# Performance work log

Measured on AMD Instinct MI355X. Metric: run time of the kernel, lower is better.

The kernel has to match this reference:

```python
import jax, jax.numpy as jnp
import numpy as np
from jax import lax

FREQ, TIME = 8, 8
TSLOTS, NUM_AP = 8, 4
N_DEV = 8192
E_DD, E_DA, E_AD = 262144, 32768, 32768
HID = 64


def _w(key, shape):
    fan_in = shape[0] if len(shape) == 2 else int(np.prod(shape[1:]))
    return jax.random.normal(key, shape, jnp.float32) / np.sqrt(fan_in)


def setup_inputs() -> dict:
    key = jax.random.key(0)
    ks = iter(jax.random.split(key, 64))
    inp = {}
    inp['device_pos'] = jax.random.normal(next(ks), (N_DEV, 2), jnp.float32)
    inp['ap_pos'] = jax.random.normal(next(ks), (NUM_AP, 2), jnp.float32)
    inp['csi'] = jax.random.normal(next(ks), (N_DEV, NUM_AP, FREQ, TIME, 2), jnp.float32)
    inp['node_packets'] = jax.random.randint(next(ks), (N_DEV,), 0, 100, jnp.int32)
    inp['dd_src'] = jax.random.randint(next(ks), (E_DD,), 0, N_DEV, jnp.int32)
    inp['dd_dst'] = jax.random.randint(next(ks), (E_DD,), 0, N_DEV, jnp.int32)
    inp['da_src'] = jax.random.randint(next(ks), (E_DA,), 0, N_DEV, jnp.int32)
    inp['da_dst'] = jax.random.randint(next(ks), (E_DA,), 0, NUM_AP, jnp.int32)
    inp['ad_src'] = jax.random.randint(next(ks), (E_AD,), 0, NUM_AP, jnp.int32)
    inp['ad_dst'] = jax.random.randint(next(ks), (E_AD,), 0, N_DEV, jnp.int32)
    # CSIEncoder params
    inp['cnn1_W'] = _w(next(ks), (16, 2, 3, 3)); inp['cnn1_b'] = jnp.zeros((16,), jnp.float32)
    inp['cnn2_W'] = _w(next(ks), (32, 16, 3, 3)); inp['cnn2_b'] = jnp.zeros((32,), jnp.float32)
    inp['csi_fc_W'] = _w(next(ks), (32 * FREQ * TIME, HID)); inp['csi_fc_b'] = jnp.zeros((HID,), jnp.float32)
    # DeviceEncoder params
    inp['dev_pos_W'] = _w(next(ks), (3, 16)); inp['dev_pos_b'] = jnp.zeros((16,), jnp.float32)
    inp['dev_csi_W'] = _w(next(ks), (NUM_AP * HID, 64)); inp['dev_csi_b'] = jnp.zeros((64,), jnp.float32)
    inp['dev_merge_W'] = _w(next(ks), (80, 64)); inp['dev_merge_b'] = jnp.zeros((64,), jnp.float32)
    # APEncoder params
    inp['ap_enc_W'] = _w(next(ks), (2, 64)); inp['ap_enc_b'] = jnp.zeros((64,), jnp.float32)
    # 2 hetero layers x 3 relations GraphConv(64,64)
    for name in ['g1_dd', 'g1_da', 'g1_ad', 'g2_dd', 'g2_da', 'g2_ad']:
        inp[name + '_W'] = _w(next(ks), (64, 64))
        inp[name + '_b'] = jnp.zeros((64,), jnp.float32)
    # ap_head (sched_head is defined but unused in the original forward)
    inp['aph1_W'] = _w(next(ks), (64, 64)); inp['aph1_b'] = jnp.zeros((64,), jnp.float32)
    inp['aph2_W'] = _w(next(ks), (64, TSLOTS * NUM_AP)); inp['aph2_b'] = jnp.zeros((TSLOTS * NUM_AP,), jnp.float32)
    return inp


def _conv2d(x, W, b):
    y = lax.conv_general_dilated(x, W, (1, 1), 'SAME', dimension_numbers=('NCHW', 'OIHW', 'NCHW'))
    return y + b[None, :, None, None]


def _graph_conv(x_src, src, dst, n_src, n_dst, W, b):
    # DGL GraphConv, norm='both': x/sqrt(out_deg) -> scatter-sum -> /sqrt(in_deg) -> linear
    ones = jnp.ones(src.shape[0], x_src.dtype)
    deg_out = jnp.maximum(jax.ops.segment_sum(ones, src, num_segments=n_src), 1.0)
    deg_in = jnp.maximum(jax.ops.segment_sum(ones, dst, num_segments=n_dst), 1.0)
    m = (x_src * lax.rsqrt(deg_out)[:, None])[src]            # gather per edge
    agg = jax.ops.segment_sum(m, dst, num_segments=n_dst)      # scatter-sum to dst
    agg = agg * lax.rsqrt(deg_in)[:, None]
    return agg @ W + b


def reference(device_pos, ap_pos, csi, node_packets, dd_src, dd_dst, da_src, da_dst, ad_src, ad_dst,
              cnn1_W, cnn1_b, cnn2_W, cnn2_b, csi_fc_W, csi_fc_b,
              dev_pos_W, dev_pos_b, dev_csi_W, dev_csi_b, dev_merge_W, dev_merge_b,
              ap_enc_W, ap_enc_b,
              g1_dd_W, g1_dd_b, g1_da_W, g1_da_b, g1_ad_W, g1_ad_b,
              g2_dd_W, g2_dd_b, g2_da_W, g2_da_b, g2_ad_W, g2_ad_b,
              aph1_W, aph1_b, aph2_W, aph2_b):
    N, AP = csi.shape[0], csi.shape[1]
    # CSIEncoder (per-AP loop vectorized as a single batched conv over N*AP)
    x = csi.reshape(N * AP, FREQ, TIME, 2).transpose(0, 3, 1, 2)   # [N*AP,2,F,T]
    x = jax.nn.relu(_conv2d(x, cnn1_W, cnn1_b))
    x = jax.nn.relu(_conv2d(x, cnn2_W, cnn2_b))
    x = x.reshape(N * AP, -1)                                      # [N*AP, 32*F*T]
    csi_embed = jax.nn.relu(x @ csi_fc_W + csi_fc_b).reshape(N, AP * HID)
    # DeviceEncoder
    pin = jnp.concatenate([device_pos, node_packets.astype(jnp.float32)[:, None]], axis=1)
    pos_f = jax.nn.relu(pin @ dev_pos_W + dev_pos_b)
    csi_f = jax.nn.relu(csi_embed @ dev_csi_W + dev_csi_b)
    h_dev = jax.nn.relu(jnp.concatenate([pos_f, csi_f], axis=1) @ dev_merge_W + dev_merge_b)
    # APEncoder
    h_ap = jax.nn.relu(ap_pos @ ap_enc_W + ap_enc_b)
    # HeteroGraphConv layer 1 (aggregate='sum' across relations sharing dst type)
    hd1 = (_graph_conv(h_dev, dd_src, dd_dst, N, N, g1_dd_W, g1_dd_b)
           + _graph_conv(h_ap, ad_src, ad_dst, NUM_AP, N, g1_ad_W, g1_ad_b))
    ha1 = _graph_conv(h_dev, da_src, da_dst, N, NUM_AP, g1_da_W, g1_da_b)
    hd1, ha1 = jax.nn.relu(hd1), jax.nn.relu(ha1)
    # HeteroGraphConv layer 2
    hd2 = (_graph_conv(hd1, dd_src, dd_dst, N, N, g2_dd_W, g2_dd_b)
           + _graph_conv(ha1, ad_src, ad_dst, NUM_AP, N, g2_ad_W, g2_ad_b))
    hd2 = jax.nn.relu(hd2)
    # ap_head -> [N, T, A]
    ap_logits = (jax.nn.relu(hd2 @ aph1_W + aph1_b) @ aph2_W + aph2_b).reshape(N, TSLOTS, NUM_AP)
    logits_AP = ap_logits.transpose(2, 1, 0)                       # [A,T,N]
    # eval branch: deterministic softmax + argmax one-hot over devices
    ap_soft_AP = jax.nn.softmax(logits_AP, axis=-1)
    idx = jnp.argmax(logits_AP, axis=-1)                           # [A,T]
    ap_onehot_AP = jax.nn.one_hot(idx, N, dtype=logits_AP.dtype)   # [A,T,N]
    ap_onehot_final = ap_onehot_AP.transpose(2, 1, 0)              # [N,T,A]
    sched_soft = ap_soft_AP.sum(axis=0).T                          # [N,T]
    sched_hard = (ap_onehot_final.sum(axis=-1) > 0).astype(jnp.float32)
    return (sched_hard, ap_logits, sched_soft)
```

## Files before the change

kernel.cpp:

```cpp
#include <hip/hip_runtime.h>

#define NDEV 8192
#define NAP  4
#define NSAMP 32768
#define EDD 262144
#define EDA 32768
#define EAD 32768
#define KC 128
#define ASTR2 132

typedef float vf2 __attribute__((ext_vector_type(2)));
static __device__ __forceinline__ vf2 pk_fma(vf2 a, vf2 b, vf2 c) {
    return __builtin_elementwise_fma(a, b, c);
}

using sh8 = __attribute__((ext_vector_type(8))) short;
using f32x4 = __attribute__((ext_vector_type(4))) float;
using f32x16 = __attribute__((ext_vector_type(16))) float;

static __device__ __forceinline__ unsigned short bf16_rtne(float f) {
    unsigned u = __float_as_uint(f);
    u += 0x7fffu + ((u >> 16) & 1u);
    return (unsigned short)(u >> 16);
}
static __device__ __forceinline__ float bf16f(unsigned short h) {
    return __uint_as_float(((unsigned)h) << 16);
}

__global__ void repack_kernel(const float* __restrict__ w2, float* __restrict__ wpk,
                              const float* __restrict__ w1, float* __restrict__ w1p,
                              const float* __restrict__ fcW, uint4* __restrict__ wfc,
                              const float* __restrict__ Wc, uint4* __restrict__ wcc)
{
    int i = blockIdx.x * 256 + threadIdx.x;
    if (i < 1152) {
        int lane = i & 63, s = (i >> 6) & 1, tap = i >> 7;
        int oc = lane & 31, g = lane >> 5;
        unsigned int d[4];
        #pragma unroll
        for (int d4 = 0; d4 < 4; ++d4) {
            unsigned short u01[2];
            #pragma unroll
            for (int h = 0; h < 2; ++h) {
                int e = 2 * d4 + h;
                int ic = g * 8 + e;
                float v = w2[oc * 144 + ic * 9 + tap];
                unsigned short hi = bf16_rtne(v);
                u01[h] = (s == 0) ? hi : bf16_rtne(v - bf16f(hi));
            }
            d[d4] = (unsigned)u01[0] | ((unsigned)u01[1] << 16);
        }
        ((uint4*)wpk)[i] = make_uint4(d[0], d[1], d[2], d[3]);
    }
    int j = i - 4608;
    if (j >= 0 && j < 288) {
        int h = j & 1, v = j >> 1;
        int o2 = v & 7, r = v >> 3;
        w1p[j] = w1[(2 * o2 + h) * 18 + r];
    }
    int h1 = i - 5120;
    if (h1 >= 0 && h1 < 32768) {
        int s = h1 & 1, l = (h1 >> 1) & 63, nt = (h1 >> 7) & 3, kstep = h1 >> 9;
        unsigned int d[4];
        #pragma unroll
        for (int d4 = 0; d4 < 4; ++d4) {
            unsigned short u01[2];
            #pragma unroll
            for (int hh = 0; hh < 2; ++hh) {
                int e = 2 * d4 + hh;
                int kp = kstep * 32 + (l >> 4) * 8 + e;
                int korig = (kp & 31) * 64 + (kp >> 5);
                int n = nt * 16 + (l & 15);
                float v = fcW[(long)korig * 64 + n];
                unsigned short hi = bf16_rtne(v);
                u01[hh] = (s == 0) ? hi : bf16_rtne(v - bf16f(hi));
            }
            d[d4] = (unsigned)u01[0] | ((unsigned)u01[1] << 16);
        }
        wfc[h1] = make_uint4(d[0], d[1], d[2], d[3]);
    }
    int h2 = i - 37888;
    if (h2 >= 0 && h2 < 4096) {
        int s = h2 & 1, l = (h2 >> 1) & 63, nt = (h2 >> 7) & 3, kstep = h2 >> 9;
        unsigned int d[4];
        #pragma unroll
        for (int d4 = 0; d4 < 4; ++d4) {
            unsigned short u01[2];
            #pragma unroll
            for (int hh = 0; hh < 2; ++hh) {
                int e = 2 * d4 + hh;
                int k = kstep * 32 + (l >> 4) * 8 + e;
                int n = nt * 16 + (l & 15);
                float v = Wc[(long)k * 64 + n];
                unsigned short hi = bf16_rtne(v);
                u01[hh] = (s == 0) ? hi : bf16_rtne(v - bf16f(hi));
            }
            d[d4] = (unsigned)u01[0] | ((unsigned)u01[1] << 16);
        }
        wcc[h2] = make_uint4(d[0], d[1], d[2], d[3]);
    }
}

#define C2STR 2052
__global__ __launch_bounds__(512) void convfc_kernel(
    const float* __restrict__ csi,
    const float* __restrict__ w1p, const float* __restrict__ b1,
    const float* __restrict__ wpk, const float* __restrict__ b2,
    const uint4* __restrict__ wfc, const float* __restrict__ fcb,
    float* __restrict__ emb)
{
    __shared__ __align__(16) char smem[135680];
    __shared__ float sw1p[288];
    __shared__ float sb1[16];
    __shared__ float sb2[32];
    __shared__ float sbF[64];
    float* inpad = (float*)smem;
    unsigned short* c1h = (unsigned short*)(smem + 12800);
    float* c2h = (float*)smem;
    float* red = (float*)smem;
    const int tid = threadIdx.x;
    const int lane = tid & 63;
    const int w = __builtin_amdgcn_readfirstlane(tid >> 6);

    for (int i = tid; i < 288; i += 512) sw1p[i] = w1p[i];
    if (tid < 16) sb1[tid] = b1[tid];
    if (tid < 32) sb2[tid] = b2[tid];
    if (tid < 64) sbF[tid] = fcb[tid];
    {
        const uint4 z4 = make_uint4(0u, 0u, 0u, 0u);
        uint4* ip4 = (uint4*)inpad;
        for (int i = tid; i < 800; i += 512) ip4[i] = z4;
        uint4* c14 = (uint4*)c1h;
        for (int i = tid; i < 15360; i += 512) c14[i] = z4;
    }
    __syncthreads();

    const long s0 = (long)blockIdx.x * 16;
    for (int i = tid; i < 2048; i += 512) {
        int si = i >> 7, r = i & 127;
        int f = r >> 4, t = (r >> 1) & 7, c = r & 1;
        inpad[si * 200 + c * 100 + (f + 1) * 10 + (t + 1)] = csi[s0 * 128 + i];
    }
    __syncthreads();

    #pragma unroll
    for (int it = 0; it < 2; ++it) {
        const int si1 = it * 8 + w;
        const int p1 = lane;
        const int f1 = p1 >> 3, t1 = p1 & 7;
        float inv[18];
        #pragma unroll
        for (int ic = 0; ic < 2; ++ic)
            #pragma unroll
            for (int df = 0; df < 3; ++df)
                #pragma unroll
                for (int dt = 0; dt < 3; ++dt)
                    inv[ic * 9 + df * 3 + dt] =
                        inpad[si1 * 200 + ic * 100 + (f1 + df) * 10 + (t1 + dt)];
        vf2 a1[8];
        #pragma unroll
        for (int o2 = 0; o2 < 8; ++o2) a1[o2] = (vf2){sb1[2 * o2], sb1[2 * o2 + 1]};
        const vf2* sw1v = (const vf2*)sw1p;
        #pragma unroll
        for (int r = 0; r < 18; ++r) {
            vf2 xv = {inv[r], inv[r]};
            #pragma unroll
            for (int o2 = 0; o2 < 8; ++o2)
                a1[o2] = pk_fma(xv, sw1v[r * 8 + o2], a1[o2]);
        }
        float v[16];
        #pragma unroll
        for (int o2 = 0; o2 < 8; ++o2) {
            v[2 * o2]     = fmaxf(a1[o2].x, 0.f);
            v[2 * o2 + 1] = fmaxf(a1[o2].y, 0.f);
        }
        const int cell = ((f1 + 1) * 12 + (t1 + 1)) * 8;
        #pragma unroll
        for (int g = 0; g < 2; ++g) {
            unsigned int hd[4], ld[4];
            #pragma unroll
            for (int d = 0; d < 4; ++d) {
                float x0 = v[g * 8 + 2 * d], x1 = v[g * 8 + 2 * d + 1];
                unsigned short h0 = bf16_rtne(x0), h1 = bf16_rtne(x1);
                unsigned short l0 = bf16_rtne(x0 - bf16f(h0));
                unsigned short l1 = bf16_rtne(x1 - bf16f(h1));
                hd[d] = (unsigned)h0 | ((unsigned)h1 << 16);
                ld[d] = (unsigned)l0 | ((unsigned)l1 << 16);
            }
            *(uint4*)&c1h[(si1 * 4 + g) * 960 + cell]     = make_uint4(hd[0], hd[1], hd[2], hd[3]);
            *(uint4*)&c1h[(si1 * 4 + 2 + g) * 960 + cell] = make_uint4(ld[0], ld[1], ld[2], ld[3]);
        }
    }

    sh8 Bh[9], Bl[9];
    {
        const sh8* bfp = (const sh8*)wpk;
        #pragma unroll
        for (int tap = 0; tap < 9; ++tap) {
            Bh[tap] = bfp[(tap * 2 + 0) * 64 + lane];
            Bl[tap] = bfp[(tap * 2 + 1) * 64 + lane];
        }
    }
    __syncthreads();

    const int rr = lane & 31, g = lane >> 5;
    const float bias2 = sb2[rr];
    const int p0f = rr >> 3, pt = rr & 7;
    const int p1f = 4 + p0f;
    #pragma unroll
    for (int q = 0; q < 2; ++q) {
        const int s = q * 8 + w;
        f32x16 acc0, acc1;
        #pragma unroll
        for (int u = 0; u < 16; ++u) { acc0[u] = bias2; acc1[u] = bias2; }
        const int hb = (s * 4 + g) * 960;
        const int lb = (s * 4 + 2 + g) * 960;
        #pragma unroll
        for (int df = 0; df < 3; ++df) {
            #pragma unroll
            for (int dt = 0; dt < 3; ++dt) {
                const int tap = df * 3 + dt;
                const int c0 = ((p0f + df) * 12 + (pt + dt)) * 8;
                const int c1i = ((p1f + df) * 12 + (pt + dt)) * 8;
                sh8 Ah0 = *(const sh8*)&c1h[hb + c0];
                sh8 Al0 = *(const sh8*)&c1h[lb + c0];
                sh8 Ah1 = *(const sh8*)&c1h[hb + c1i];
                sh8 Al1 = *(const sh8*)&c1h[lb + c1i];
                acc0 = __builtin_amdgcn_mfma_f32_32x32x16_bf16(Ah0, Bh[tap], acc0, 0, 0, 0);
                acc1 = __builtin_amdgcn_mfma_f32_32x32x16_bf16(Ah1, Bh[tap], acc1, 0, 0, 0);
                acc0 = __builtin_amdgcn_mfma_f32_32x32x16_bf16(Ah0, Bl[tap], acc0, 0, 0, 0);
                acc1 = __builtin_amdgcn_mfma_f32_32x32x16_bf16(Ah1, Bl[tap], acc1, 0, 0, 0);
                acc0 = __builtin_amdgcn_mfma_f32_32x32x16_bf16(Al0, Bh[tap], acc0, 0, 0, 0);
                acc1 = __builtin_amdgcn_mfma_f32_32x32x16_bf16(Al1, Bh[tap], acc1, 0, 0, 0);
            }
        }
        __syncthreads();
        float* crow = c2h + (size_t)s * C2STR;
        #pragma unroll
        for (int i = 0; i < 16; ++i) {
            const int pos = (i & 3) + 8 * (i >> 2) + 4 * g;
            crow[pos * 32 + rr]        = fmaxf(acc0[i], 0.f);
            crow[(pos + 32) * 32 + rr] = fmaxf(acc1[i], 0.f);
        }
    }
    __syncthreads();

    const int ks = w;
    const int mrow = lane & 15;
    const int g2 = lane >> 4;
    f32x4 acc[4];
    #pragma unroll
    for (int nt = 0; nt < 4; ++nt) acc[nt] = (f32x4){0.f, 0.f, 0.f, 0.f};
    #pragma unroll 2
    for (int t = 0; t < 8; ++t) {
        const int kstep = ks * 8 + t;
        const uint4* bp = wfc + (size_t)kstep * 512 + lane * 2;
        uint4 bh0 = bp[0],   bl0 = bp[1];
        uint4 bh1 = bp[128], bl1 = bp[129];
        uint4 bh2 = bp[256], bl2 = bp[257];
        uint4 bh3 = bp[384], bl3 = bp[385];
        const float4 a0 = *(const float4*)&c2h[mrow * C2STR + kstep * 32 + g2 * 8];
        const float4 a1 = *(const float4*)&c2h[mrow * C2STR + kstep * 32 + g2 * 8 + 4];
        float av[8] = {a0.x, a0.y, a0.z, a0.w, a1.x, a1.y, a1.z, a1.w};
        unsigned short hs[8], lss[8];
        #pragma unroll
        for (int e = 0; e < 8; ++e) {
            hs[e] = bf16_rtne(av[e]);
            lss[e] = bf16_rtne(av[e] - bf16f(hs[e]));
        }
        sh8 Ah = {(short)hs[0], (short)hs[1], (short)hs[2], (short)hs[3],
                  (short)hs[4], (short)hs[5], (short)hs[6], (short)hs[7]};
        sh8 Al = {(short)lss[0], (short)lss[1], (short)lss[2], (short)lss[3],
                  (short)lss[4], (short)lss[5], (short)lss[6], (short)lss[7]};
        #define FCMM(ntv, bhv, blv) \
            acc[ntv] = __builtin_amdgcn_mfma_f32_16x16x32_bf16(Ah, *(const sh8*)&(bhv), acc[ntv], 0, 0, 0); \
            acc[ntv] = __builtin_amdgcn_mfma_f32_16x16x32_bf16(Ah, *(const sh8*)&(blv), acc[ntv], 0, 0, 0); \
            acc[ntv] = __builtin_amdgcn_mfma_f32_16x16x32_bf16(Al, *(const sh8*)&(bhv), acc[ntv], 0, 0, 0);
        FCMM(0, bh0, bl0)
        FCMM(1, bh1, bl1)
        FCMM(2, bh2, bl2)
        FCMM(3, bh3, bl3)
        #undef FCMM
    }
    __syncthreads();
    #pragma unroll
    for (int nt = 0; nt < 4; ++nt)
        #pragma unroll
        for (int r = 0; r < 4; ++r)
            red[(ks * 16 + g2 * 4 + r) * 64 + nt * 16 + mrow] = acc[nt][r];
    __syncthreads();
    if (tid < 256) {
        const int m = tid >> 4, oq = tid & 15;
        float4 sum;
        sum.x = sbF[oq * 4 + 0]; sum.y = sbF[oq * 4 + 1];
        sum.z = sbF[oq * 4 + 2]; sum.w = sbF[oq * 4 + 3];
        #pragma unroll
        for (int jq = 0; jq < 8; ++jq) {
            float4 rv = *(float4*)&red[(jq * 16 + m) * 64 + oq * 4];
            sum.x += rv.x; sum.y += rv.y; sum.z += rv.z; sum.w += rv.w;
        }
        float4 o4;
        o4.x = fmaxf(sum.x, 0.f); o4.y = fmaxf(sum.y, 0.f);
        o4.z = fmaxf(sum.z, 0.f); o4.w = fmaxf(sum.w, 0.f);
        *(float4*)&emb[(s0 + m) * 64 + oq * 4] = o4;
    }
}

__global__ __launch_bounds__(256) void fc16_kernel(
    const float* __restrict__ A, const uint4* __restrict__ Wfrag,
    const float* __restrict__ bias, float* __restrict__ out, int K)
{
    __shared__ __align__(16) float smem[4224];
    float* As = smem;
    const int tid = threadIdx.x;
    const long m0g = (long)blockIdx.x * 16;
    const int ks = tid >> 6;
    const int lane = tid & 63;
    const int mrow = lane & 15;
    const int g = lane >> 4;

    f32x4 acc[4];
    #pragma unroll
    for (int nt = 0; nt < 4; ++nt) acc[nt] = (f32x4){0.f, 0.f, 0.f, 0.f};

    for (int kc = 0; kc < K; kc += KC) {
        __syncthreads();
        #pragma unroll
        for (int i = 0; i < 2; ++i) {
            int idx = tid + i * 256;
            int m = idx >> 5, kq = idx & 31;
            float4 v = *(const float4*)&A[(m0g + m) * K + kc + kq * 4];
            *(float4*)&As[m * ASTR2 + kq * 4] = v;
        }
        __syncthreads();
        const int kstep = (kc >> 5) + ks;
        const uint4* bp = Wfrag + (size_t)kstep * 512 + lane * 2;
        uint4 bh0 = bp[0],   bl0 = bp[1];
        uint4 bh1 = bp[128], bl1 = bp[129];
        uint4 bh2 = bp[256], bl2 = bp[257];
        uint4 bh3 = bp[384], bl3 = bp[385];
        const float4 a0 = *(const float4*)&As[mrow * ASTR2 + ks * 32 + g * 8];
        const float4 a1 = *(const float4*)&As[mrow * ASTR2 + ks * 32 + g * 8 + 4];
        float av[8] = {a0.x, a0.y, a0.z, a0.w, a1.x, a1.y, a1.z, a1.w};
        unsigned short hs[8], lss[8];
        #pragma unroll
        for (int e = 0; e < 8; ++e) {
            hs[e] = bf16_rtne(av[e]);
            lss[e] = bf16_rtne(av[e] - bf16f(hs[e]));
        }
        sh8 Ah = {(short)hs[0], (short)hs[1], (short)hs[2], (short)hs[3],
                  (short)hs[4], (short)hs[5], (short)hs[6], (short)hs[7]};
        sh8 Al = {(short)lss[0], (short)lss[1], (short)lss[2], (short)lss[3],
                  (short)lss[4], (short)lss[5], (short)lss[6], (short)lss[7]};
        #define FCMM(ntv, bhv, blv) \
            acc[ntv] = __builtin_amdgcn_mfma_f32_16x16x32_bf16(Ah, *(const sh8*)&(bhv), acc[ntv], 0, 0, 0); \
            acc[ntv] = __builtin_amdgcn_mfma_f32_16x16x32_bf16(Ah, *(const sh8*)&(blv), acc[ntv], 0, 0, 0); \
            acc[ntv] = __builtin_amdgcn_mfma_f32_16x16x32_bf16(Al, *(const sh8*)&(bhv), acc[ntv], 0, 0, 0);
        FCMM(0, bh0, bl0)
        FCMM(1, bh1, bl1)
        FCMM(2, bh2, bl2)
        FCMM(3, bh3, bl3)
        #undef FCMM
    }
    __syncthreads();
    float* red = smem;
    #pragma unroll
    for (int nt = 0; nt < 4; ++nt)
        #pragma unroll
        for (int r = 0; r < 4; ++r)
            red[(ks * 16 + g * 4 + r) * 64 + nt * 16 + mrow] = acc[nt][r];
    __syncthreads();
    {
        int m = tid >> 4, oq = tid & 15;
        float4 r0 = *(float4*)&red[(0 * 16 + m) * 64 + oq * 4];
        float4 r1 = *(float4*)&red[(1 * 16 + m) * 64 + oq * 4];
        float4 r2 = *(float4*)&red[(2 * 16 + m) * 64 + oq * 4];
        float4 r3 = *(float4*)&red[(3 * 16 + m) * 64 + oq * 4];
        const float4 b4 = *(const float4*)&bias[oq * 4];
        float4 o4;
        o4.x = fmaxf(r0.x + r1.x + r2.x + r3.x + b4.x, 0.f);
        o4.y = fmaxf(r0.y + r1.y + r2.y + r3.y + b4.y, 0.f);
        o4.z = fmaxf(r0.z + r1.z + r2.z + r3.z + b4.z, 0.f);
        o4.w = fmaxf(r0.w + r1.w + r2.w + r3.w + b4.w, 0.f);
        *(float4*)&out[(m0g + m) * 64 + oq * 4] = o4;
    }
}

__global__ __launch_bounds__(256) void merge_kernel(
    const float* __restrict__ dpos, const int* __restrict__ pkts,
    const float* __restrict__ csif,
    const float* __restrict__ Wp, const float* __restrict__ bp,
    const float* __restrict__ Wm, const float* __restrict__ bm,
    const int* __restrict__ degout,
    float* __restrict__ hdev, float* __restrict__ xn,
    const float* __restrict__ appos, const float* __restrict__ Wap,
    const float* __restrict__ bap, const int* __restrict__ degapo,
    float* __restrict__ hap, float* __restrict__ xnap)
{
    __shared__ float sWm[80][64];
    __shared__ float spos[4][16];
    __shared__ float scf[4][64];
    const int tid = threadIdx.x;
    for (int i = tid; i < 5120; i += 256) sWm[i >> 6][i & 63] = Wm[i];
    const int n0 = blockIdx.x * 4;
    (&scf[0][0])[tid] = csif[(long)n0 * 64 + tid];
    if (tid < 64) {
        int dl = tid >> 4, o = tid & 15;
        int d = n0 + dl;
        float px = dpos[d * 2], py = dpos[d * 2 + 1], pk = (float)pkts[d];
        float v = bp[o] + px * Wp[o] + py * Wp[16 + o] + pk * Wp[32 + o];
        spos[dl][o] = fmaxf(v, 0.f);
    }
    __syncthreads();
    const int o = tid & 63, dl = tid >> 6;
    float h = bm[o];
    #pragma unroll
    for (int j = 0; j < 16; ++j) h += spos[dl][j] * sWm[j][o];
    #pragma unroll 8
    for (int j = 0; j < 64; ++j) h += scf[dl][j] * sWm[16 + j][o];
    h = fmaxf(h, 0.f);
    const long idx = (long)(n0 + dl) * 64 + o;
    hdev[idx] = h;
    xn[idx] = h * rsqrtf(fmaxf((float)degout[n0 + dl], 1.f));
    if (blockIdx.x == 0) {
        int a = tid >> 6, oo = tid & 63;
        float v = fmaxf(bap[oo] + appos[a * 2] * Wap[oo] + appos[a * 2 + 1] * Wap[64 + oo], 0.f);
        hap[tid] = v;
        xnap[tid] = v * rsqrtf(fmaxf((float)degapo[a], 1.f));
    }
}

__global__ __launch_bounds__(256) void degrees_kernel(
    const int* __restrict__ dd_src, const int* __restrict__ dd_dst,
    const int* __restrict__ da_src, const int* __restrict__ da_dst,
    const int* __restrict__ ad_src, const int* __restrict__ ad_dst,
    int* deg_dd_out, int* deg_dd_in, int* deg_da_out, int* deg_ad_in, int* deg_small)
{
    __shared__ int s4[16];
    const int tid = threadIdx.x;
    if (tid < 16) s4[tid] = 0;
    __syncthreads();
    const int gid = blockIdx.x * 256 + tid;
    atomicAdd(&deg_dd_out[dd_src[gid]], 1);
    atomicAdd(&deg_dd_in[dd_dst[gid]], 1);
    if (gid < EDA) {
        atomicAdd(&deg_da_out[da_src[gid]], 1);
        atomicAdd(&s4[da_dst[gid]], 1);
        atomicAdd(&s4[8 + ad_src[gid]], 1);
        atomicAdd(&deg_ad_in[ad_dst[gid]], 1);
    }
    __syncthreads();
    if (tid < 16 && s4[tid] != 0) atomicAdd(&deg_small[tid], s4[tid]);
}

__global__ __launch_bounds__(1024) void scan_kernel(
    const int* __restrict__ degA, int* rsA, int* curA,
    const int* __restrict__ degB, int* rsB, int* curB)
{
    const int* deg = blockIdx.x ? degB : degA;
    int* rs = blockIdx.x ? rsB : rsA;
    int* cur = blockIdx.x ? curB : curA;
    __shared__ int sd[1024];
    const int tid = threadIdx.x;
    const int base = tid * 8;
    int v[8]; int s = 0;
    #pragma unroll
    for (int j = 0; j < 8; ++j) { v[j] = deg[base + j]; s += v[j]; }
    sd[tid] = s;
    __syncthreads();
    for (int off = 1; off < 1024; off <<= 1) {
        int t = (tid >= off) ? sd[tid - off] : 0;
        __syncthreads();
        sd[tid] += t;
        __syncthreads();
    }
    int ex = sd[tid] - s;
    #pragma unroll
    for (int j = 0; j < 8; ++j) { rs[base + j] = ex; cur[base + j] = ex; ex += v[j]; }
}

__global__ __launch_bounds__(256) void reorder_kernel(
    const int* __restrict__ src, const int* __restrict__ dst,
    int* __restrict__ cursor, int* __restrict__ ssrc, int nE)
{
    int e = blockIdx.x * 256 + threadIdx.x;
    if (e < nE) {
        int pos = atomicAdd(&cursor[dst[e]], 1);
        ssrc[pos] = src[e];
    }
}

__global__ __launch_bounds__(256) void gatherx_kernel(
    const int* __restrict__ rsdd, const int* __restrict__ degddi,
    const int* __restrict__ ssdd, const float* __restrict__ xn, float* __restrict__ aggdd,
    const int* __restrict__ rsad, const int* __restrict__ degadi,
    const int* __restrict__ ssad, const float* __restrict__ xnap, float* __restrict__ aggad,
    const int* __restrict__ da_src, const int* __restrict__ da_dst,
    const float* __restrict__ hdev, const int* __restrict__ degdao,
    float* __restrict__ aggda)
{
    __shared__ float sacc[4][64];
    const int b = blockIdx.x;
    const int tid = threadIdx.x;
    if (b < 1024) {
        const bool isdd = b < 512;
        const int lane = tid & 63;
        const int gbase = lane & 48;
        const int lg = lane & 15;
        const int fq = lg * 4;
        const int d = (isdd ? b : b - 512) * 16 + (tid >> 4);
        const int* rs = isdd ? rsdd : rsad;
        const int* dg = isdd ? degddi : degadi;
        const int* ss = isdd ? ssdd : ssad;
        const float* x = isdd ? xn : xnap;
        float* agg = isdd ? aggdd : aggad;
        const int start = rs[d], len = dg[d];
        float ax = 0.f, ay = 0.f, az = 0.f, aw = 0.f;
        for (int j = 0; j < len; j += 16) {
            const int rem = min(16, len - j);
            const int myidx = ss[start + j + min(lg, rem - 1)];
            float4 v[16];
            #pragma unroll
            for (int k = 0; k < 16; ++k) {
                const int sk = __shfl(myidx, gbase + min(k, rem - 1), 64);
                v[k] = *(const float4*)&x[(long)sk * 64 + fq];
            }
            #pragma unroll
            for (int k = 0; k < 16; ++k) {
                const float m = (k < rem) ? 1.f : 0.f;
                ax += m * v[k].x; ay += m * v[k].y;
                az += m * v[k].z; aw += m * v[k].w;
            }
        }
        const float sc = rsqrtf(fmaxf((float)len, 1.f));
        float4 o;
        o.x = ax * sc; o.y = ay * sc; o.z = az * sc; o.w = aw * sc;
        *(float4*)&agg[(long)d * 64 + fq] = o;
    } else {
        (&sacc[0][0])[tid] = 0.f;
        __syncthreads();
        const int f = tid & 63;
        const int base = (b - 1024) * 128;
        for (int e = base + (tid >> 6); e < base + 128; e += 4) {
            int s = da_src[e], d = da_dst[e];
            float sc = rsqrtf(fmaxf((float)degdao[s], 1.f));
            atomicAdd(&sacc[d][f], hdev[(long)s * 64 + f] * sc);
        }
        __syncthreads();
        float v = (&sacc[0][0])[tid];
        if (v != 0.f) atomicAdd(&aggda[tid], v);
    }
}

__global__ __launch_bounds__(256) void combinex_kernel(
    const float* __restrict__ agg1, const float* __restrict__ W1, const float* __restrict__ b1,
    const float* __restrict__ agg2, const float* __restrict__ W2, const float* __restrict__ b2,
    const int* __restrict__ degout, float* __restrict__ out, float* __restrict__ xnout,
    const float* __restrict__ aggda, const int* __restrict__ degdai,
    const float* __restrict__ Wda, const float* __restrict__ bda,
    const int* __restrict__ degapo, float* __restrict__ ha_out, float* __restrict__ ha_xn)
{
    __shared__ float sW1[64][64];
    __shared__ float sW2[64][64];
    __shared__ float sa1[4][64];
    __shared__ float sa2[4][64];
    const int tid = threadIdx.x;
    if (blockIdx.x < 2048) {
        for (int i = tid; i < 4096; i += 256) { sW1[i >> 6][i & 63] = W1[i]; sW2[i >> 6][i & 63] = W2[i]; }
        const int n0 = blockIdx.x * 4;
        (&sa1[0][0])[tid] = agg1[(long)n0 * 64 + tid];
        (&sa2[0][0])[tid] = agg2[(long)n0 * 64 + tid];
        __syncthreads();
        const int o = tid & 63, dl = tid >> 6;
        float acc1 = 0.f, acc2 = 0.f;
        #pragma unroll 8
        for (int k = 0; k < 64; ++k) {
            acc1 += sa1[dl][k] * sW1[k][o];
            acc2 += sa2[dl][k] * sW2[k][o];
        }
        float h = fmaxf(acc1 + acc2 + b1[o] + b2[o], 0.f);
        const long idx = (long)(n0 + dl) * 64 + o;
        out[idx] = h;
        if (xnout) xnout[idx] = h * rsqrtf(fmaxf((float)degout[n0 + dl], 1.f));
    } else {
        const int o = tid & 63, a = tid >> 6;
        float acc = 0.f;
        for (int k = 0; k < 64; ++k) acc += aggda[a * 64 + k] * Wda[k * 64 + o];
        float r = rsqrtf(fmaxf((float)degdai[a], 1.f));
        float h = fmaxf(acc * r + bda[o], 0.f);
        ha_out[tid] = h;
        ha_xn[tid] = h * rsqrtf(fmaxf((float)degapo[a], 1.f));
    }
}

__global__ __launch_bounds__(256) void head_kernel(
    const float* __restrict__ hd2,
    const float* __restrict__ W1, const float* __restrict__ b1,
    const float* __restrict__ W2, const float* __restrict__ b2,
    float* __restrict__ logits_out)
{
    __shared__ float sW1[64][64];
    __shared__ float sW2[64][32];
    __shared__ float sh[4][64];
    __shared__ float st[4][64];
    const int tid = threadIdx.x;
    for (int i = tid; i < 4096; i += 256) sW1[i >> 6][i & 63] = W1[i];
    for (int i = tid; i < 2048; i += 256) sW2[i >> 5][i & 31] = W2[i];
    const int n0 = blockIdx.x * 4;
    (&sh[0][0])[tid] = hd2[(long)n0 * 64 + tid];
    __syncthreads();
    const int o = tid & 63, dl = tid >> 6;
    float acc = b1[o];
    #pragma unroll 8
    for (int k = 0; k < 64; ++k) acc += sh[dl][k] * sW1[k][o];
    st[dl][o] = fmaxf(acc, 0.f);
    __syncthreads();
    if (tid < 128) {
        int j = tid & 31, d2 = tid >> 5;
        float a2 = b2[j];
        #pragma unroll 8
        for (int k = 0; k < 64; ++k) a2 += st[d2][k] * sW2[k][j];
        logits_out[(long)(n0 + d2) * 32 + j] = a2;
    }
}

__global__ __launch_bounds__(1024) void softmax_stats_kernel(
    const float* __restrict__ logits,
    float* __restrict__ smax, int* __restrict__ sargm, float* __restrict__ ssum)
{
    __shared__ float smx[1024];
    __shared__ int sid[1024];
    __shared__ float ssm[1024];
    const int j = blockIdx.x;
    const int tid = threadIdx.x;
    float best = -__builtin_inff(); int bid = 0x7fffffff;
    for (int n = tid; n < NDEV; n += 1024) {
        float v = logits[n * 32 + j];
        if (v > best) { best = v; bid = n; }
    }
    smx[tid] = best; sid[tid] = bid;
    __syncthreads();
    for (int s = 512; s > 0; s >>= 1) {
        if (tid < s) {
            float v2 = smx[tid + s]; int i2 = sid[tid + s];
            if (v2 > smx[tid] || (v2 == smx[tid] && i2 < sid[tid])) { smx[tid] = v2; sid[tid] = i2; }
        }
        __syncthreads();
    }
    const float mx = smx[0];
    float part = 0.f;
    for (int n = tid; n < NDEV; n += 1024) part += expf(logits[n * 32 + j] - mx);
    ssm[tid] = part;
    __syncthreads();
    for (int s = 512; s > 0; s >>= 1) {
        if (tid < s) ssm[tid] += ssm[tid + s];
        __syncthreads();
    }
    if (tid == 0) { smax[j] = mx; sargm[j] = sid[0]; ssum[j] = ssm[0]; }
}

__global__ __launch_bounds__(256) void final_kernel(
    const float* __restrict__ logits, const float* __restrict__ smax,
    const int* __restrict__ sargm, const float* __restrict__ ssum,
    float* __restrict__ hard, float* __restrict__ soft)
{
    const int gid = blockIdx.x * 256 + threadIdx.x;
    const int n = gid >> 3, t = gid & 7;
    float s = 0.f; int h = 0;
    #pragma unroll
    for (int a = 0; a < 4; ++a) {
        int j = t * 4 + a;
        s += expf(logits[n * 32 + j] - smax[j]) / ssum[j];
        h |= (sargm[j] == n) ? 1 : 0;
    }
    hard[gid] = (float)h;
    soft[gid] = s;
}

extern "C" void kernel_launch(void* const* d_in, const int* in_sizes, int n_in,
                              void* d_out, int out_size, void* d_ws, size_t ws_size,
                              hipStream_t stream)
{
    const float* device_pos = (const float*)d_in[0];
    const float* ap_pos     = (const float*)d_in[1];
    const float* csi        = (const float*)d_in[2];
    const int*   node_pk    = (const int*)d_in[3];
    const int* dd_src = (const int*)d_in[4];
    const int* dd_dst = (const int*)d_in[5];
    const int* da_src = (const int*)d_in[6];
    const int* da_dst = (const int*)d_in[7];
    const int* ad_src = (const int*)d_in[8];
    const int* ad_dst = (const int*)d_in[9];
    const float* w1  = (const float*)d_in[10]; const float* b1  = (const float*)d_in[11];
    const float* w2  = (const float*)d_in[12]; const float* b2  = (const float*)d_in[13];
    const float* fcW = (const float*)d_in[14]; const float* fcb = (const float*)d_in[15];
    const float* Wp  = (const float*)d_in[16]; const float* bp  = (const float*)d_in[17];
    const float* Wc  = (const float*)d_in[18]; const float* bc  = (const float*)d_in[19];
    const float* Wm  = (const float*)d_in[20]; const float* bm  = (const float*)d_in[21];
    const float* Wap = (const float*)d_in[22]; const float* bap = (const float*)d_in[23];
    const float* g1ddW = (const float*)d_in[24]; const float* g1ddb = (const float*)d_in[25];
    const float* g1daW = (const float*)d_in[26]; const float* g1dab = (const float*)d_in[27];
    const float* g1adW = (const float*)d_in[28]; const float* g1adb = (const float*)d_in[29];
    const float* g2ddW = (const float*)d_in[30]; const float* g2ddb = (const float*)d_in[31];
    const float* g2adW = (const float*)d_in[34]; const float* g2adb = (const float*)d_in[35];
    const float* a1W = (const float*)d_in[36]; const float* a1b = (const float*)d_in[37];
    const float* a2W = (const float*)d_in[38]; const float* a2b = (const float*)d_in[39];

    float* ws = (float*)d_ws;
    size_t o_emb   = 0;
    size_t o_csif  = o_emb + (size_t)NSAMP * 64;
    size_t o_hdev  = o_csif + (size_t)NDEV * 64;
    size_t o_hap   = o_hdev + (size_t)NDEV * 64;
    size_t o_hd1   = o_hap + 256;
    size_t o_ha1   = o_hd1 + (size_t)NDEV * 64;
    size_t o_hd2   = o_ha1 + 256;
    size_t o_aggdd = o_hd2 + (size_t)NDEV * 64;
    size_t o_aggad = o_aggdd + (size_t)NDEV * 64;
    size_t o_xn    = o_aggad + (size_t)NDEV * 64;
    size_t o_xnap  = o_xn + (size_t)NDEV * 64;
    size_t o_wpk   = o_xnap + 256;
    size_t o_w1p   = o_wpk + 4608;
    size_t o_wfc   = o_w1p + 288;
    size_t o_wcc   = o_wfc + 131072;
    size_t o_zero  = o_wcc + 16384;
    size_t o_degddo = o_zero;
    size_t o_degddi = o_degddo + NDEV;
    size_t o_degdao = o_degddi + NDEV;
    size_t o_degadi = o_degdao + NDEV;
    size_t o_degsm  = o_degadi + NDEV;
    size_t o_aggda  = o_degsm + 16;
    size_t o_zend   = o_aggda + 256;
    size_t o_rsdd  = o_zend;
    size_t o_curdd = o_rsdd + NDEV;
    size_t o_rsad  = o_curdd + NDEV;
    size_t o_curad = o_rsad + NDEV;
    size_t o_ssdd  = o_curad + NDEV;
    size_t o_ssad  = o_ssdd + EDD;
    size_t o_smax  = o_ssad + EAD;
    size_t o_ssum  = o_smax + 32;
    size_t o_sargm = o_ssum + 32;

    float* out = (float*)d_out;
    float* out_hard   = out;
    float* out_logits = out + 65536;
    float* out_soft   = out + 65536 + 262144;

    hipMemsetAsync((void*)(ws + o_zero), 0, (o_zend - o_zero) * sizeof(float), stream);
    repack_kernel<<<164, 256, 0, stream>>>(w2, ws + o_wpk, w1, ws + o_w1p,
                                           fcW, (uint4*)(ws + o_wfc),
                                           Wc, (uint4*)(ws + o_wcc));

    degrees_kernel<<<EDD / 256, 256, 0, stream>>>(dd_src, dd_dst, da_src, da_dst, ad_src, ad_dst,
                                                  (int*)(ws + o_degddo), (int*)(ws + o_degddi),
                                                  (int*)(ws + o_degdao), (int*)(ws + o_degadi),
                                                  (int*)(ws + o_degsm));
    scan_kernel<<<2, 1024, 0, stream>>>((int*)(ws + o_degddi), (int*)(ws + o_rsdd), (int*)(ws + o_curdd),
                                        (int*)(ws + o_degadi), (int*)(ws + o_rsad), (int*)(ws + o_curad));
    reorder_kernel<<<EDD / 256, 256, 0, stream>>>(dd_src, dd_dst, (int*)(ws + o_curdd),
                                                  (int*)(ws + o_ssdd), EDD);
    reorder_kernel<<<EAD / 256, 256, 0, stream>>>(ad_src, ad_dst, (int*)(ws + o_curad),
                                                  (int*)(ws + o_ssad), EAD);

    convfc_kernel<<<NSAMP / 16, 512, 0, stream>>>(csi, ws + o_w1p, b1, ws + o_wpk, b2,
                                                  (const uint4*)(ws + o_wfc), fcb, ws + o_emb);

    fc16_kernel<<<NDEV / 16, 256, 0, stream>>>(ws + o_emb, (const uint4*)(ws + o_wcc),
                                               bc, ws + o_csif, 256);
    merge_kernel<<<NDEV / 4, 256, 0, stream>>>(device_pos, node_pk, ws + o_csif,
                                               Wp, bp, Wm, bm, (int*)(ws + o_degddo),
                                               ws + o_hdev, ws + o_xn,
                                               ap_pos, Wap, bap, (int*)(ws + o_degsm) + 8,
                                               ws + o_hap, ws + o_xnap);

    gatherx_kernel<<<1280, 256, 0, stream>>>((int*)(ws + o_rsdd), (int*)(ws + o_degddi),
                                             (int*)(ws + o_ssdd), ws + o_xn, ws + o_aggdd,
                                             (int*)(ws + o_rsad), (int*)(ws + o_degadi),
                                             (int*)(ws + o_ssad), ws + o_xnap, ws + o_aggad,
                                             da_src, da_dst, ws + o_hdev,
                                             (int*)(ws + o_degdao), ws + o_aggda);
    combinex_kernel<<<2049, 256, 0, stream>>>(ws + o_aggdd, g1ddW, g1ddb,
                                              ws + o_aggad, g1adW, g1adb,
                                              (int*)(ws + o_degddo), ws + o_hd1, ws + o_xn,
                                              ws + o_aggda, (int*)(ws + o_degsm),
                                              g1daW, g1dab, (int*)(ws + o_degsm) + 8,
                                              ws + o_ha1, ws + o_xnap);

    gatherx_kernel<<<1024, 256, 0, stream>>>((int*)(ws + o_rsdd), (int*)(ws + o_degddi),
                                             (int*)(ws + o_ssdd), ws + o_xn, ws + o_aggdd,
                                             (int*)(ws + o_rsad), (int*)(ws + o_degadi),
                                             (int*)(ws + o_ssad), ws + o_xnap, ws + o_aggad,
                                             da_src, da_dst, ws + o_hd1,
                                             (int*)(ws + o_degdao), ws + o_aggda);
    combinex_kernel<<<2048, 256, 0, stream>>>(ws + o_aggdd, g2ddW, g2ddb,
                                              ws + o_aggad, g2adW, g2adb,
                                              (int*)(ws + o_degddo), ws + o_hd2, nullptr,
                                              nullptr, nullptr, nullptr, nullptr,
                                              nullptr, nullptr, nullptr);

    head_kernel<<<NDEV / 4, 256, 0, stream>>>(ws + o_hd2, a1W, a1b, a2W, a2b, out_logits);

    softmax_stats_kernel<<<32, 1024, 0, stream>>>(out_logits, ws + o_smax,
                                                  (int*)(ws + o_sargm), ws + o_ssum);
    final_kernel<<<65536 / 256, 256, 0, stream>>>(out_logits, ws + o_smax,
                                                  (int*)(ws + o_sargm), ws + o_ssum,
                                                  out_hard, out_soft);
    (void)in_sizes; (void)n_in; (void)out_size; (void)ws_size;
}
```

Baseline: 434.7 us.

## Double convfc block to 1024 threads, one sample per wave, split FC N-tiles

The fused conv/FC kernel now runs with 1024 threads (16 waves) per block. Each wave handles one of the 16 samples in conv1 and conv2 instead of looping over two. The FC stage splits the four N-tiles across wave halves, so each wave holds two accumulators. This is meant to expose more wave-level parallelism and latency hiding within a block, at the cost of a tighter register budget per thread under the 1024 launch bound (the conv2 stage keeps 18 B fragments live) and heavier barrier synchronisation.

```diff
diff --git a/kernel.cpp b/kernel.cpp
--- a/kernel.cpp
+++ b/kernel.cpp
@@ -102,7 +102,7 @@
 }
 
 #define C2STR 2052
-__global__ __launch_bounds__(512) void convfc_kernel(
+__global__ __launch_bounds__(1024) void convfc_kernel(
     const float* __restrict__ csi,
     const float* __restrict__ w1p, const float* __restrict__ b1,
     const float* __restrict__ wpk, const float* __restrict__ b2,
@@ -122,30 +122,29 @@
     const int lane = tid & 63;
     const int w = __builtin_amdgcn_readfirstlane(tid >> 6);
 
-    for (int i = tid; i < 288; i += 512) sw1p[i] = w1p[i];
+    for (int i = tid; i < 288; i += 1024) sw1p[i] = w1p[i];
     if (tid < 16) sb1[tid] = b1[tid];
     if (tid < 32) sb2[tid] = b2[tid];
     if (tid < 64) sbF[tid] = fcb[tid];
     {
         const uint4 z4 = make_uint4(0u, 0u, 0u, 0u);
         uint4* ip4 = (uint4*)inpad;
-        for (int i = tid; i < 800; i += 512) ip4[i] = z4;
+        for (int i = tid; i < 800; i += 1024) ip4[i] = z4;
         uint4* c14 = (uint4*)c1h;
-        for (int i = tid; i < 15360; i += 512) c14[i] = z4;
+        for (int i = tid; i < 15360; i += 1024) c14[i] = z4;
     }
     __syncthreads();
 
     const long s0 = (long)blockIdx.x * 16;
-    for (int i = tid; i < 2048; i += 512) {
+    for (int i = tid; i < 2048; i += 1024) {
         int si = i >> 7, r = i & 127;
         int f = r >> 4, t = (r >> 1) & 7, c = r & 1;
         inpad[si * 200 + c * 100 + (f + 1) * 10 + (t + 1)] = csi[s0 * 128 + i];
     }
     __syncthreads();
 
-    #pragma unroll
-    for (int it = 0; it < 2; ++it) {
-        const int si1 = it * 8 + w;
+    {
+        const int si1 = w;
         const int p1 = lane;
         const int f1 = p1 >> 3, t1 = p1 & 7;
         float inv[18];
@@ -207,9 +206,8 @@
     const float bias2 = sb2[rr];
     const int p0f = rr >> 3, pt = rr & 7;
     const int p1f = 4 + p0f;
-    #pragma unroll
-    for (int q = 0; q < 2; ++q) {
-        const int s = q * 8 + w;
+    {
+        const int s = w;
         f32x16 acc0, acc1;
         #pragma unroll
         for (int u = 0; u < 16; ++u) { acc0[u] = bias2; acc1[u] = bias2; }
@@ -245,20 +243,19 @@
     }
     __syncthreads();
 
-    const int ks = w;
+    const int ks = w & 7;
+    const int ntb = (w >> 3) * 2;
     const int mrow = lane & 15;
     const int g2 = lane >> 4;
-    f32x4 acc[4];
+    f32x4 acc[2];
     #pragma unroll
-    for (int nt = 0; nt < 4; ++nt) acc[nt] = (f32x4){0.f, 0.f, 0.f, 0.f};
-    #pragma unroll 2
+    for (int ni = 0; ni < 2; ++ni) acc[ni] = (f32x4){0.f, 0.f, 0.f, 0.f};
+    #pragma unroll
     for (int t = 0; t < 8; ++t) {
         const int kstep = ks * 8 + t;
         const uint4* bp = wfc + (size_t)kstep * 512 + lane * 2;
-        uint4 bh0 = bp[0],   bl0 = bp[1];
-        uint4 bh1 = bp[128], bl1 = bp[129];
-        uint4 bh2 = bp[256], bl2 = bp[257];
-        uint4 bh3 = bp[384], bl3 = bp[385];
+        uint4 bh0 = bp[ntb * 128],       bl0 = bp[ntb * 128 + 1];
+        uint4 bh1 = bp[(ntb + 1) * 128], bl1 = bp[(ntb + 1) * 128 + 1];
         const float4 a0 = *(const float4*)&c2h[mrow * C2STR + kstep * 32 + g2 * 8];
         const float4 a1 = *(const float4*)&c2h[mrow * C2STR + kstep * 32 + g2 * 8 + 4];
         float av[8] = {a0.x, a0.y, a0.z, a0.w, a1.x, a1.y, a1.z, a1.w};
@@ -272,22 +269,21 @@
                   (short)hs[4], (short)hs[5], (short)hs[6], (short)hs[7]};
         sh8 Al = {(short)lss[0], (short)lss[1], (short)lss[2], (short)lss[3],
                   (short)lss[4], (short)lss[5], (short)lss[6], (short)lss[7]};
-        #define FCMM(ntv, bhv, blv) \
-            acc[ntv] = __builtin_amdgcn_mfma_f32_16x16x32_bf16(Ah, *(const sh8*)&(bhv), acc[ntv], 0, 0, 0); \
-            acc[ntv] = __builtin_amdgcn_mfma_f32_16x16x32_bf16(Ah, *(const sh8*)&(blv), acc[ntv], 0, 0, 0); \
-            acc[ntv] = __builtin_amdgcn_mfma_f32_16x16x32_bf16(Al, *(const sh8*)&(bhv), acc[ntv], 0, 0, 0);
-        FCMM(0, bh0, bl0)
-        FCMM(1, bh1, bl1)
-        FCMM(2, bh2, bl2)
-        FCMM(3, bh3, bl3)
-        #undef FCMM
+        acc[0] = __builtin_amdgcn_mfma_f32_16x16x32_bf16(Ah, *(const sh8*)&bh0, acc[0], 0, 0, 0);
+        acc[0] = __builtin_amdgcn_mfma_f32_16x16x32_bf16(Ah, *(const sh8*)&bl0, acc[0], 0, 0, 0);
+        acc[0] = __builtin_amdgcn_mfma_f32_16x16x32_bf16(Al, *(const sh8*)&bh0, acc[0], 0, 0, 0);
+        acc[1] = __builtin_amdgcn_mfma_f32_16x16x32_bf16(Ah, *(const sh8*)&bh1, acc[1], 0, 0, 0);
+        acc[1] = __builtin_amdgcn_mfma_f32_16x16x32_bf16(Ah, *(const sh8*)&bl1, acc[1], 0, 0, 0);
+        acc[1] = __builtin_amdgcn_mfma_f32_16x16x32_bf16(Al, *(const sh8*)&bh1, acc[1], 0, 0, 0);
     }
     __syncthreads();
     #pragma unroll
-    for (int nt = 0; nt < 4; ++nt)
+    for (int ni = 0; ni < 2; ++ni) {
+        const int nt = ntb + ni;
         #pragma unroll
         for (int r = 0; r < 4; ++r)
-            red[(ks * 16 + g2 * 4 + r) * 64 + nt * 16 + mrow] = acc[nt][r];
+            red[(ks * 16 + g2 * 4 + r) * 64 + nt * 16 + mrow] = acc[ni][r];
+    }
     __syncthreads();
     if (tid < 256) {
         const int m = tid >> 4, oq = tid & 15;
@@ -761,8 +757,8 @@
     reorder_kernel<<<EAD / 256, 256, 0, stream>>>(ad_src, ad_dst, (int*)(ws + o_curad),
                                                   (int*)(ws + o_ssad), EAD);
 
-    convfc_kernel<<<NSAMP / 16, 512, 0, stream>>>(csi, ws + o_w1p, b1, ws + o_wpk, b2,
-                                                  (const uint4*)(ws + o_wfc), fcb, ws + o_emb);
+    convfc_kernel<<<NSAMP / 16, 1024, 0, stream>>>(csi, ws + o_w1p, b1, ws + o_wpk, b2,
+                                                   (const uint4*)(ws + o_wfc), fcb, ws + o_emb);
 
     fc16_kernel<<<NDEV / 16, 256, 0, stream>>>(ws + o_emb, (const uint4*)(ws + o_wcc),
                                                bc, ws + o_csif, 256);
```

Result: no change. 436.0 us (+0.3%).
